# Performance work log

Measured on AMD Instinct MI355X. Metric: run time of the kernel, lower is better.

Reference implementation:

```python
import jax, jax.numpy as jnp
import numpy as np

N, E, C, L, H = 32768, 524288, 128, 3, 4
B, S = 64, 512            # graphs, nodes per graph (N = B*S, equal-size graphs)
F_X, F_PE = 64, 16
IN_DIM = F_X + F_PE
HID, OUT = 256, 1
EPS = 1e-5                # BatchNorm1d eps
HD = C // H               # head dim


def setup_inputs():
    key = jax.random.key(0)
    ks = iter(jax.random.split(key, 32))
    rn = lambda shape, s=0.05: jax.random.normal(next(ks), shape, dtype=jnp.float32) * s
    return dict(
        x=jax.random.normal(next(ks), (N, F_X), dtype=jnp.float32),
        pe=jax.random.normal(next(ks), (N, F_PE), dtype=jnp.float32),
        edge_index=jax.random.randint(next(ks), (2, E), 0, N),
        batch=jnp.repeat(jnp.arange(B), S),
        W_emb=rn((IN_DIM, C)), b_emb=jnp.zeros((C,), jnp.float32),
        gcn_w=rn((L, C, C)), gcn_b=jnp.zeros((L, C), jnp.float32),
        in_w=rn((L, 3 * C, C)), in_b=jnp.zeros((L, 3 * C), jnp.float32),
        out_w=rn((L, C, C)), out_b=jnp.zeros((L, C), jnp.float32),
        mlp_w1=rn((L, C, 2 * C)), mlp_b1=jnp.zeros((L, 2 * C), jnp.float32),
        mlp_w2=rn((L, 2 * C, C)), mlp_b2=jnp.zeros((L, C), jnp.float32),
        g1=jnp.ones((L, C), jnp.float32), be1=jnp.zeros((L, C), jnp.float32),
        g2=jnp.ones((L, C), jnp.float32), be2=jnp.zeros((L, C), jnp.float32),
        g3=jnp.ones((L, C), jnp.float32), be3=jnp.zeros((L, C), jnp.float32),
        W_hid=rn((C, HID)), b_hid=jnp.zeros((HID,), jnp.float32),
        W_out=rn((HID, OUT)), b_out=jnp.zeros((OUT,), jnp.float32),
    )


def _bn(h, g, b):
    # BatchNorm1d over nodes (training-mode batch stats, biased var)
    mu = h.mean(0)
    var = h.var(0)
    return (h - mu) * jax.lax.rsqrt(var + EPS) * g + b


def _gelu(x):
    return jax.nn.gelu(x, approximate=False)  # torch F.gelu default is erf


def reference(x, pe, edge_index, batch, W_emb, b_emb, gcn_w, gcn_b, in_w, in_b,
              out_w, out_b, mlp_w1, mlp_b1, mlp_w2, mlp_b2, g1, be1, g2, be2,
              g3, be3, W_hid, b_hid, W_out, b_out):
    # GCN normalization with self-loops (computed once; topology fixed)
    loops = jnp.arange(N)
    src = jnp.concatenate([edge_index[0], loops])
    dst = jnp.concatenate([edge_index[1], loops])
    deg = jax.ops.segment_sum(jnp.ones_like(src, jnp.float32), dst, num_segments=N)
    dinv = jnp.where(deg > 0, jax.lax.rsqrt(deg), 0.0)
    coef = (dinv[src] * dinv[dst])[:, None]

    h = jnp.concatenate([x, pe], axis=-1) @ W_emb + b_emb  # [N,C]
    scale = jnp.asarray(1.0 / np.sqrt(HD), jnp.float32)

    for l in range(L):
        # --- local GCNConv + residual + BN ---
        xw = h @ gcn_w[l]
        loc = jax.ops.segment_sum(xw[src] * coef, dst, num_segments=N) + gcn_b[l]
        h1 = _bn(loc + h, g1[l], be1[l])
        # --- global multihead attention on dense batch [B,S,C] ---
        hd = h.reshape(B, S, C)
        qkv = hd @ in_w[l].T + in_b[l]
        q, k, v = jnp.split(qkv, 3, axis=-1)
        sh = lambda t: t.reshape(B, S, H, HD).transpose(0, 2, 1, 3)  # [B,H,S,HD]
        q, k, v = sh(q), sh(k), sh(v)
        att = jax.nn.softmax(jnp.einsum('bhqd,bhkd->bhqk', q, k) * scale, axis=-1)
        ao = jnp.einsum('bhqk,bhkd->bhqd', att, v).transpose(0, 2, 1, 3).reshape(N, C)
        ao = ao @ out_w[l].T + out_b[l]
        h2 = _bn(ao + h, g2[l], be2[l])
        # --- combine + MLP residual + BN, then outer GELU ---
        out = h1 + h2
        m = jax.nn.relu(out @ mlp_w1[l] + mlp_b1[l]) @ mlp_w2[l] + mlp_b2[l]
        h = _gelu(_bn(out + m, g3[l], be3[l]))

    # global mean pool over graphs
    cnt = jax.ops.segment_sum(jnp.ones((N,), jnp.float32), batch, num_segments=B)
    pooled = jax.ops.segment_sum(h, batch, num_segments=B) / cnt[:, None]
    z = _gelu(pooled @ W_hid + b_hid)
    return (z @ W_out + b_out).squeeze()  # [B]
```

## Files before the change

kernel.cpp:

```cpp
#include <hip/hip_runtime.h>
#include <hip/hip_bf16.h>
#include <math.h>

#define NNODES 32768
#define NEDGES 524288
#define CCH 128
#define NLAYERS 3
#define NHEADS 4
#define HDIM 32
#define NB_GRAPH 64
#define SNODES 512
#define INDIM 80
#define HIDDEN 256
#define BNEPS 1e-5f

typedef _Float16 f16;
typedef f16 half8_t __attribute__((ext_vector_type(8)));
typedef f16 half4_t __attribute__((ext_vector_type(4)));
typedef float float4_t __attribute__((ext_vector_type(4)));

__device__ __forceinline__ float gelu_f(float x) {
    return 0.5f * x * (1.0f + erff(x * 0.70710678118654752f));
}

__global__ void k_count(const int* __restrict__ dst, int* __restrict__ deg) {
    int e = blockIdx.x * blockDim.x + threadIdx.x;
    if (e < NEDGES) atomicAdd(&deg[dst[e]], 1);
}

__global__ void k_dinv_from_deg(const int* __restrict__ deg, float* __restrict__ dinv) {
    int i = blockIdx.x * blockDim.x + threadIdx.x;
    if (i < NNODES) dinv[i] = rsqrtf((float)(deg[i] + 1));
}

__global__ __launch_bounds__(1024) void k_scan(const int* __restrict__ deg,
                                               int* __restrict__ rowptr,
                                               int* __restrict__ cursor) {
    __shared__ int sa[1024], sb[1024];
    int t = threadIdx.x;
    int base = t * 32;
    int local[32];
    int s = 0;
    #pragma unroll
    for (int i = 0; i < 32; i++) { local[i] = s; s += deg[base + i]; }
    sa[t] = s;
    __syncthreads();
    int* sp = sa; int* dp = sb;
    for (int off = 1; off < 1024; off <<= 1) {
        dp[t] = (t >= off) ? sp[t] + sp[t - off] : sp[t];
        __syncthreads();
        int* tmp = sp; sp = dp; dp = tmp;
    }
    int excl = (t == 0) ? 0 : sp[t - 1];
    #pragma unroll
    for (int i = 0; i < 32; i++) {
        int v = excl + local[i];
        rowptr[base + i] = v;
        cursor[base + i] = v;
    }
    if (t == 1023) rowptr[NNODES] = sp[1023];
}

__global__ void k_fill_edges(const int* __restrict__ src, const int* __restrict__ dst,
                             int* __restrict__ cursor, int* __restrict__ col) {
    int e = blockIdx.x * blockDim.x + threadIdx.x;
    if (e >= NEDGES) return;
    int pos = atomicAdd(&cursor[dst[e]], 1);
    col[pos] = src[e];
}

__global__ void k_concat(const float* __restrict__ x, const float* __restrict__ pe,
                         float* __restrict__ out) {
    int gid = blockIdx.x * blockDim.x + threadIdx.x;
    if (gid >= NNODES * 32) return;
    int n = gid >> 5, q = gid & 31;
    float4 v = {0.f, 0.f, 0.f, 0.f};
    if (q < 16)      v = ((const float4*)x)[(size_t)n * 16 + q];
    else if (q < 20) v = ((const float4*)pe)[(size_t)n * 4 + (q - 16)];
    ((float4*)out)[gid] = v;
}

__global__ void k_wconv(const float* __restrict__ src, f16* __restrict__ hi,
                        f16* __restrict__ lo, int Nn, int Ks, int Kp, int trans,
                        int L, int ostride) {
    int gid = blockIdx.x * blockDim.x + threadIdx.x;
    int per = Nn * Kp;
    if (gid >= per * L) return;
    int l = gid / per, r = gid % per;
    int n = r / Kp, k = r % Kp;
    float v = 0.f;
    if (k < Ks)
        v = trans ? src[(size_t)l * Nn * Ks + (size_t)n * Ks + k]
                  : src[(size_t)l * Ks * Nn + (size_t)k * Nn + n];
    f16 h = (f16)v;
    size_t o = (size_t)l * ostride + r;
    hi[o] = h;
    lo[o] = (f16)(v - (float)h);
}

template<int ACT, bool SPLIT>
__global__ __launch_bounds__(256) void k_gemm_mfma(
        const float* __restrict__ A, const f16* __restrict__ Whi,
        const f16* __restrict__ Wlo, const float* __restrict__ bias,
        const float* __restrict__ rowscale, float* __restrict__ C,
        int M, int N, int K, float* __restrict__ C2,
        const float* __restrict__ bias2) {
    __shared__ f16 Ah[128 * 40];
    __shared__ f16 Al[128 * 40];
    __shared__ f16 Bh[128 * 40];
    __shared__ f16 Bl[128 * 40];
    const int t = threadIdx.x;
    const int bm = blockIdx.y * 128, bn = blockIdx.x * 128;
    const int w = t >> 6, lane = t & 63;
    const int g = lane >> 4, q = lane & 15;

    float4_t acc[2][8];
    #pragma unroll
    for (int mt = 0; mt < 2; mt++)
        #pragma unroll
        for (int nt = 0; nt < 8; nt++)
            acc[mt][nt] = (float4_t){0.f, 0.f, 0.f, 0.f};

    const int srow = t >> 1, shf = (t & 1) * 16;

    for (int kc = 0; kc < K; kc += 32) {
        {
            const float* ap = A + (size_t)(bm + srow) * K + kc + shf;
            float va[16];
            *(float4*)&va[0]  = ((const float4*)ap)[0];
            *(float4*)&va[4]  = ((const float4*)ap)[1];
            *(float4*)&va[8]  = ((const float4*)ap)[2];
            *(float4*)&va[12] = ((const float4*)ap)[3];
            half8_t h0, h1, l0, l1;
            #pragma unroll
            for (int j = 0; j < 8; j++) {
                f16 h = (f16)va[j];
                h0[j] = h; l0[j] = (f16)(va[j] - (float)h);
            }
            #pragma unroll
            for (int j = 0; j < 8; j++) {
                f16 h = (f16)va[8 + j];
                h1[j] = h; l1[j] = (f16)(va[8 + j] - (float)h);
            }
            *(half8_t*)&Ah[srow * 40 + shf]     = h0;
            *(half8_t*)&Ah[srow * 40 + shf + 8] = h1;
            *(half8_t*)&Al[srow * 40 + shf]     = l0;
            *(half8_t*)&Al[srow * 40 + shf + 8] = l1;
        }
        {
            const f16* bp = Whi + (size_t)(bn + srow) * K + kc + shf;
            *(half8_t*)&Bh[srow * 40 + shf]     = ((const half8_t*)bp)[0];
            *(half8_t*)&Bh[srow * 40 + shf + 8] = ((const half8_t*)bp)[1];
            const f16* lp = Wlo + (size_t)(bn + srow) * K + kc + shf;
            *(half8_t*)&Bl[srow * 40 + shf]     = ((const half8_t*)lp)[0];
            *(half8_t*)&Bl[srow * 40 + shf + 8] = ((const half8_t*)lp)[1];
        }
        __syncthreads();

        half8_t ah[2], al[2];
        #pragma unroll
        for (int mt = 0; mt < 2; mt++) {
            ah[mt] = *(half8_t*)&Ah[(w * 32 + mt * 16 + q) * 40 + g * 8];
            al[mt] = *(half8_t*)&Al[(w * 32 + mt * 16 + q) * 40 + g * 8];
        }
        #pragma unroll
        for (int nt = 0; nt < 8; nt++) {
            half8_t bh = *(half8_t*)&Bh[(nt * 16 + q) * 40 + g * 8];
            half8_t bl = *(half8_t*)&Bl[(nt * 16 + q) * 40 + g * 8];
            #pragma unroll
            for (int mt = 0; mt < 2; mt++) {
                acc[mt][nt] = __builtin_amdgcn_mfma_f32_16x16x32_f16(ah[mt], bh, acc[mt][nt], 0, 0, 0);
                acc[mt][nt] = __builtin_amdgcn_mfma_f32_16x16x32_f16(al[mt], bh, acc[mt][nt], 0, 0, 0);
                acc[mt][nt] = __builtin_amdgcn_mfma_f32_16x16x32_f16(ah[mt], bl, acc[mt][nt], 0, 0, 0);
            }
        }
        __syncthreads();
    }

    #pragma unroll
    for (int mt = 0; mt < 2; mt++) {
        #pragma unroll
        for (int r = 0; r < 4; r++) {
            int row = bm + w * 32 + mt * 16 + 4 * g + r;
            if constexpr (SPLIT) {
                if (blockIdx.x == 0) {
                    float rs = rowscale[row];
                    #pragma unroll
                    for (int nt = 0; nt < 8; nt++) {
                        int cn = bn + nt * 16 + q;
                        C[(size_t)row * 128 + cn] = acc[mt][nt][r] * rs;
                    }
                } else {
                    #pragma unroll
                    for (int nt = 0; nt < 8; nt++) {
                        int cn2 = bn - 128 + nt * 16 + q;
                        C2[(size_t)row * 384 + cn2] = acc[mt][nt][r] + bias2[cn2];
                    }
                }
            } else {
                float rs = rowscale ? rowscale[row] : 1.0f;
                #pragma unroll
                for (int nt = 0; nt < 8; nt++) {
                    int cn = bn + nt * 16 + q;
                    float v = acc[mt][nt][r] + (bias ? bias[cn] : 0.0f);
                    v *= rs;
                    if (ACT == 1) v = fmaxf(v, 0.0f);
                    C[(size_t)row * N + cn] = v;
                }
            }
        }
    }
}

__global__ __launch_bounds__(256) void k_gcn_gather(
        const int* __restrict__ rowptr, const int* __restrict__ col,
        const float* __restrict__ xws, const float* __restrict__ dinv,
        const float* __restrict__ bias, float* __restrict__ loc) {
    int t = threadIdx.x;
    int node = blockIdx.x * 8 + (t >> 5);
    int q = t & 31;
    int r0 = rowptr[node], r1 = rowptr[node + 1];
    float4 acc = ((const float4*)(xws + (size_t)node * CCH))[q];
    for (int j = r0; j < r1; j++) {
        int s = col[j];
        float4 v = ((const float4*)(xws + (size_t)s * CCH))[q];
        acc.x += v.x; acc.y += v.y; acc.z += v.z; acc.w += v.w;
    }
    float dv = dinv[node];
    float4 b4 = ((const float4*)bias)[q];
    float4 o;
    o.x = fmaf(acc.x, dv, b4.x); o.y = fmaf(acc.y, dv, b4.y);
    o.z = fmaf(acc.z, dv, b4.z); o.w = fmaf(acc.w, dv, b4.w);
    ((float4*)(loc + (size_t)node * CCH))[q] = o;
}

__global__ __launch_bounds__(256) void k_bn_stats(const float* __restrict__ a,
                                                  const float* __restrict__ b,
                                                  float* __restrict__ part) {
    __shared__ float s1[256], s2[256];
    int t = threadIdx.x, blk = blockIdx.x;
    int c = t & 127, half = t >> 7;
    float sum = 0.f, sq = 0.f;
    for (int i = 0; i < 128; i++) {
        size_t r = (size_t)blk * 256 + half + 2 * i;
        float v = a[r * CCH + c] + b[r * CCH + c];
        sum += v;
        sq = fmaf(v, v, sq);
    }
    s1[t] = sum; s2[t] = sq;
    __syncthreads();
    if (t < 128) {
        part[blk * 256 + t]       = s1[t] + s1[t + 128];
        part[blk * 256 + 128 + t] = s2[t] + s2[t + 128];
    }
}

__global__ void k_bn_finalize(const float* __restrict__ part, const float* __restrict__ g,
                              const float* __restrict__ be, float* __restrict__ sc,
                              float* __restrict__ sh) {
    int c = threadIdx.x;
    float s = 0.f, sq = 0.f;
    for (int bk = 0; bk < 128; bk++) {
        s  += part[bk * 256 + c];
        sq += part[bk * 256 + 128 + c];
    }
    float mu = s / (float)NNODES;
    float var = sq / (float)NNODES - mu * mu;
    float rs = rsqrtf(var + BNEPS);
    float gg = g[c] * rs;
    sc[c] = gg;
    sh[c] = be[c] - mu * gg;
}

template<int ACT>
__global__ void k_bn_apply(const float* __restrict__ a, const float* __restrict__ b,
                           const float* __restrict__ sc, const float* __restrict__ sh,
                           float* __restrict__ out) {
    int gid = blockIdx.x * blockDim.x + threadIdx.x;
    if (gid >= NNODES * 32) return;
    int c = (gid & 31) * 4;
    float4 av = ((const float4*)a)[gid];
    float4 bv = ((const float4*)b)[gid];
    float r[4];
    float xs[4] = {av.x + bv.x, av.y + bv.y, av.z + bv.z, av.w + bv.w};
    #pragma unroll
    for (int j = 0; j < 4; j++) {
        float v = fmaf(xs[j], sc[c + j], sh[c + j]);
        if (ACT == 2) v = gelu_f(v);
        r[j] = v;
    }
    float4 o = {r[0], r[1], r[2], r[3]};
    ((float4*)out)[gid] = o;
}

__global__ void k_bn_apply_add(const float* __restrict__ a, const float* __restrict__ b,
                               const float* __restrict__ sc, const float* __restrict__ sh,
                               float* __restrict__ io) {
    int gid = blockIdx.x * blockDim.x + threadIdx.x;
    if (gid >= NNODES * 32) return;
    int c = (gid & 31) * 4;
    float4 av = ((const float4*)a)[gid];
    float4 bv = ((const float4*)b)[gid];
    float4 ov = ((const float4*)io)[gid];
    float xs[4] = {av.x + bv.x, av.y + bv.y, av.z + bv.z, av.w + bv.w};
    float r[4] = {ov.x, ov.y, ov.z, ov.w};
    #pragma unroll
    for (int j = 0; j < 4; j++) r[j] += fmaf(xs[j], sc[c + j], sh[c + j]);
    float4 o = {r[0], r[1], r[2], r[3]};
    ((float4*)io)[gid] = o;
}

__global__ __launch_bounds__(256, 1) void k_attn_mfma(const float* __restrict__ qkv,
                                                      float* __restrict__ ao) {
    __shared__ f16 Ks[512 * 40];
    __shared__ f16 VT[32 * 512];
    const int bh = blockIdx.x;
    const int b = bh >> 2, hh = bh & 3;
    const int t = threadIdx.x;
    const int lane = t & 63, wave = t >> 6;
    const int g = lane >> 4, q16 = lane & 15;
    const float scale = 0.17677669529663689f;

    const float* base = qkv + (size_t)b * SNODES * 384;

    #pragma unroll
    for (int it = 0; it < 8; it++) {
        int u = it * 256 + t;
        int row = u >> 2, c = u & 3;
        const float* gp = base + (size_t)row * 384 + CCH + hh * HDIM + c * 8;
        float4 v0 = *(const float4*)gp;
        float4 v1 = *(const float4*)(gp + 4);
        half8_t hv;
        hv[0] = (f16)v0.x; hv[1] = (f16)v0.y; hv[2] = (f16)v0.z; hv[3] = (f16)v0.w;
        hv[4] = (f16)v1.x; hv[5] = (f16)v1.y; hv[6] = (f16)v1.z; hv[7] = (f16)v1.w;
        *(half8_t*)(Ks + row * 40 + c * 8) = hv;
    }

    #pragma unroll
    for (int it = 0; it < 16; it++) {
        int j4 = (t >> 3) & 3;
        int n  = it * 32 + ((t >> 5) & 7) * 4 + j4;
        int c  = t & 7;
        float4 v = *(const float4*)(base + (size_t)n * 384 + 2 * CCH + hh * HDIM + c * 4);
        float4 u1;
        u1.x = __shfl_xor(v.x, 8); u1.y = __shfl_xor(v.y, 8);
        u1.z = __shfl_xor(v.z, 8); u1.w = __shfl_xor(v.w, 8);
        float4 w;
        if ((t & 8) == 0) { w.x = v.x;  w.y = u1.x; w.z = v.z;  w.w = u1.z; }
        else              { w.x = u1.y; w.y = v.y;  w.z = u1.w; w.w = v.w;  }
        float4 u2;
        u2.x = __shfl_xor(w.x, 16); u2.y = __shfl_xor(w.y, 16);
        u2.z = __shfl_xor(w.z, 16); u2.w = __shfl_xor(w.w, 16);
        float4 o;
        if ((t & 16) == 0) { o.x = w.x;  o.y = w.y;  o.z = u2.x; o.w = u2.y; }
        else               { o.x = u2.z; o.y = u2.w; o.z = w.z;  o.w = w.w;  }
        int hd = c * 4 + j4;
        int n0 = it * 32 + ((t >> 5) & 7) * 4;
        half4_t pk;
        pk[0] = (f16)o.x; pk[1] = (f16)o.y; pk[2] = (f16)o.z; pk[3] = (f16)o.w;
        int pos = ((n0 >> 2) + hd) & 127;
        *(half4_t*)(VT + hd * 512 + pos * 4) = pk;
    }
    __syncthreads();

    for (int j = 0; j < 8; j++) {
        int qt = wave * 8 + j;

        const float* qp = base + (size_t)(qt * 16 + q16) * 384 + hh * HDIM + g * 8;
        float4 q0 = *(const float4*)qp;
        float4 q1 = *(const float4*)(qp + 4);
        half8_t qf;
        qf[0] = (f16)(q0.x * scale); qf[1] = (f16)(q0.y * scale);
        qf[2] = (f16)(q0.z * scale); qf[3] = (f16)(q0.w * scale);
        qf[4] = (f16)(q1.x * scale); qf[5] = (f16)(q1.y * scale);
        qf[6] = (f16)(q1.z * scale); qf[7] = (f16)(q1.w * scale);

        float4_t acc[32];
        #pragma unroll
        for (int kt = 0; kt < 32; kt++) {
            half8_t kf = *(half8_t*)(Ks + (kt * 16 + q16) * 40 + g * 8);
            float4_t z = {0.f, 0.f, 0.f, 0.f};
            acc[kt] = __builtin_amdgcn_mfma_f32_16x16x32_f16(kf, qf, z, 0, 0, 0);
        }

        float m = -1e30f;
        #pragma unroll
        for (int kt = 0; kt < 32; kt++)
            m = fmaxf(m, fmaxf(fmaxf(acc[kt][0], acc[kt][1]),
                               fmaxf(acc[kt][2], acc[kt][3])));
        m = fmaxf(m, __shfl_xor(m, 16));
        m = fmaxf(m, __shfl_xor(m, 32));
        float s = 0.f;
        #pragma unroll
        for (int kt = 0; kt < 32; kt++) {
            acc[kt][0] = __expf(acc[kt][0] - m);
            acc[kt][1] = __expf(acc[kt][1] - m);
            acc[kt][2] = __expf(acc[kt][2] - m);
            acc[kt][3] = __expf(acc[kt][3] - m);
            s += acc[kt][0] + acc[kt][1] + acc[kt][2] + acc[kt][3];
        }
        s += __shfl_xor(s, 16);
        s += __shfl_xor(s, 32);
        float inv = 1.0f / s;

        half8_t pa[16];
        #pragma unroll
        for (int T = 0; T < 16; T++) {
            pa[T][0] = (f16)(acc[2 * T][0] * inv);
            pa[T][1] = (f16)(acc[2 * T][1] * inv);
            pa[T][2] = (f16)(acc[2 * T][2] * inv);
            pa[T][3] = (f16)(acc[2 * T][3] * inv);
            pa[T][4] = (f16)(acc[2 * T + 1][0] * inv);
            pa[T][5] = (f16)(acc[2 * T + 1][1] * inv);
            pa[T][6] = (f16)(acc[2 * T + 1][2] * inv);
            pa[T][7] = (f16)(acc[2 * T + 1][3] * inv);
        }

        float4_t oa0 = {0.f, 0.f, 0.f, 0.f}, oa1 = {0.f, 0.f, 0.f, 0.f};
        #pragma unroll
        for (int T = 0; T < 16; T++) {
            int hd0 = q16;
            half4_t b00 = *(half4_t*)(VT + hd0 * 512 + (((8 * T + g + hd0) & 127) * 4));
            half4_t b01 = *(half4_t*)(VT + hd0 * 512 + (((8 * T + 4 + g + hd0) & 127) * 4));
            half8_t vb0;
            vb0[0] = b00[0]; vb0[1] = b00[1]; vb0[2] = b00[2]; vb0[3] = b00[3];
            vb0[4] = b01[0]; vb0[5] = b01[1]; vb0[6] = b01[2]; vb0[7] = b01[3];
            oa0 = __builtin_amdgcn_mfma_f32_16x16x32_f16(pa[T], vb0, oa0, 0, 0, 0);
            int hd1 = 16 + q16;
            half4_t b10 = *(half4_t*)(VT + hd1 * 512 + (((8 * T + g + hd1) & 127) * 4));
            half4_t b11 = *(half4_t*)(VT + hd1 * 512 + (((8 * T + 4 + g + hd1) & 127) * 4));
            half8_t vb1;
            vb1[0] = b10[0]; vb1[1] = b10[1]; vb1[2] = b10[2]; vb1[3] = b10[3];
            vb1[4] = b11[0]; vb1[5] = b11[1]; vb1[6] = b11[2]; vb1[7] = b11[3];
            oa1 = __builtin_amdgcn_mfma_f32_16x16x32_f16(pa[T], vb1, oa1, 0, 0, 0);
        }

        #pragma unroll
        for (int r = 0; r < 4; r++) {
            size_t row = (size_t)(b * SNODES + qt * 16 + 4 * g + r);
            ao[row * CCH + hh * HDIM + q16]      = oa0[r];
            ao[row * CCH + hh * HDIM + 16 + q16] = oa1[r];
        }
    }
}

__global__ __launch_bounds__(256) void k_pool2(const float* __restrict__ h,
                                               const int* __restrict__ batch,
                                               float* __restrict__ pooled,
                                               float* __restrict__ cnt) {
    __shared__ float bins[NB_GRAPH * 132];
    __shared__ int cbin[NB_GRAPH];
    int t = threadIdx.x;
    for (int i = t; i < NB_GRAPH * 132; i += 256) bins[i] = 0.f;
    if (t < NB_GRAPH) cbin[t] = 0;
    __syncthreads();
    int n0 = blockIdx.x * 256;
    int c = t & 127, half = t >> 7;
    for (int i = 0; i < 128; i++) {
        int n = n0 + 2 * i + half;
        int g = batch[n];
        atomicAdd(&bins[g * 132 + c], h[(size_t)n * CCH + c]);
        if (c == 0) atomicAdd(&cbin[g], 1);
    }
    __syncthreads();
    for (int i = t; i < NB_GRAPH * CCH; i += 256) {
        int g = i >> 7, cc = i & 127;
        float v = bins[g * 132 + cc];
        if (v != 0.f) atomicAdd(&pooled[g * CCH + cc], v);
    }
    if (t < NB_GRAPH && cbin[t]) atomicAdd(&cnt[t], (float)cbin[t]);
}

__global__ __launch_bounds__(256) void k_head(const float* __restrict__ pooled,
                                              const float* __restrict__ cnt,
                                              const float* __restrict__ Wh,
                                              const float* __restrict__ bh,
                                              const float* __restrict__ Wo,
                                              const float* __restrict__ bo,
                                              float* __restrict__ out) {
    __shared__ float p[128];
    __shared__ float red[256];
    int g = blockIdx.x, t = threadIdx.x;
    if (t < 128) p[t] = pooled[g * CCH + t] / cnt[g];
    __syncthreads();
    float a = bh[t];
    for (int k = 0; k < 128; k++) a = fmaf(p[k], Wh[k * HIDDEN + t], a);
    float z = gelu_f(a);
    red[t] = z * Wo[t];
    __syncthreads();
    for (int s = 128; s > 0; s >>= 1) {
        if (t < s) red[t] += red[t + s];
        __syncthreads();
    }
    if (t == 0) out[g] = red[0] + bo[0];
}

extern "C" void kernel_launch(void* const* d_in, const int* in_sizes, int n_in,
                              void* d_out, int out_size, void* d_ws, size_t ws_size,
                              hipStream_t stream) {
    const float* x      = (const float*)d_in[0];
    const float* pe     = (const float*)d_in[1];
    const int*   ei     = (const int*)d_in[2];
    const int*   batch  = (const int*)d_in[3];
    const float* W_emb  = (const float*)d_in[4];
    const float* b_emb  = (const float*)d_in[5];
    const float* gcn_w  = (const float*)d_in[6];
    const float* gcn_b  = (const float*)d_in[7];
    const float* in_w   = (const float*)d_in[8];
    const float* in_b   = (const float*)d_in[9];
    const float* out_w  = (const float*)d_in[10];
    const float* out_b  = (const float*)d_in[11];
    const float* mlp_w1 = (const float*)d_in[12];
    const float* mlp_b1 = (const float*)d_in[13];
    const float* mlp_w2 = (const float*)d_in[14];
    const float* mlp_b2 = (const float*)d_in[15];
    const float* g1     = (const float*)d_in[16];
    const float* be1    = (const float*)d_in[17];
    const float* g2     = (const float*)d_in[18];
    const float* be2    = (const float*)d_in[19];
    const float* g3     = (const float*)d_in[20];
    const float* be3    = (const float*)d_in[21];
    const float* W_hid  = (const float*)d_in[22];
    const float* b_hid  = (const float*)d_in[23];
    const float* W_out  = (const float*)d_in[24];
    const float* b_out  = (const float*)d_in[25];
    float* out = (float*)d_out;

    float* ws = (float*)d_ws;
    const size_t NC = (size_t)NNODES * CCH;
    float* dinv   = ws;
    float* h      = dinv + NNODES;
    float* A      = h + NC;
    float* Bb     = A + NC;
    float* qkv    = Bb + NC;
    float* part   = qkv + (size_t)NNODES * 384;
    float* sc     = part + 128 * 256;
    float* sh     = sc + CCH;
    float* pooled = sh + CCH;
    float* cnt    = pooled + (size_t)NB_GRAPH * CCH;
    int*   ideg   = (int*)(cnt + NB_GRAPH);
    int*   rowptr = ideg + NNODES;
    int*   cursor = rowptr + NNODES + 1;
    int*   col    = cursor + NNODES;
    f16* wb    = (f16*)(col + NEDGES);
    f16* embh  = wb;                      f16* embl = embh + 128 * 128;
    f16* cwh   = embl + 128 * 128;        f16* cwl  = cwh + 3 * 512 * 128;
    f16* outh  = cwl + 3 * 512 * 128;     f16* outl = outh + 3 * 128 * 128;
    f16* m1h   = outl + 3 * 128 * 128;    f16* m1l  = m1h + 3 * 256 * 128;
    f16* m2h   = m1l + 3 * 256 * 128;     f16* m2l  = m2h + 3 * 128 * 256;

    const int* srcp = ei;
    const int* dstp = ei + NEDGES;

    const int NC4 = NNODES * 32;

    hipMemsetAsync(ideg, 0, NNODES * sizeof(int), stream);
    k_count<<<NEDGES / 256, 256, 0, stream>>>(dstp, ideg);
    k_dinv_from_deg<<<NNODES / 256, 256, 0, stream>>>(ideg, dinv);
    k_scan<<<1, 1024, 0, stream>>>(ideg, rowptr, cursor);
    k_fill_edges<<<NEDGES / 256, 256, 0, stream>>>(srcp, dstp, cursor, col);

    k_wconv<<<(128 * 128 + 255) / 256, 256, 0, stream>>>(W_emb, embh, embl, 128, 80, 128, 0, 1, 128 * 128);
    k_wconv<<<(3 * 128 * 128 + 255) / 256, 256, 0, stream>>>(gcn_w, cwh, cwl, 128, 128, 128, 0, 3, 512 * 128);
    k_wconv<<<(3 * 384 * 128 + 255) / 256, 256, 0, stream>>>(in_w, cwh + 128 * 128, cwl + 128 * 128, 384, 128, 128, 1, 3, 512 * 128);
    k_wconv<<<(3 * 128 * 128 + 255) / 256, 256, 0, stream>>>(out_w, outh, outl, 128, 128, 128, 1, 3, 128 * 128);
    k_wconv<<<(3 * 256 * 128 + 255) / 256, 256, 0, stream>>>(mlp_w1, m1h, m1l, 256, 128, 128, 0, 3, 256 * 128);
    k_wconv<<<(3 * 128 * 256 + 255) / 256, 256, 0, stream>>>(mlp_w2, m2h, m2l, 128, 256, 256, 0, 3, 128 * 256);

    k_concat<<<NC4 / 256, 256, 0, stream>>>(x, pe, A);
    k_gemm_mfma<0, false><<<dim3(1, NNODES / 128), 256, 0, stream>>>(
        A, embh, embl, b_emb, nullptr, h, NNODES, CCH, 128, nullptr, nullptr);

    for (int l = 0; l < NLAYERS; l++) {
        k_gemm_mfma<0, true><<<dim3(4, NNODES / 128), 256, 0, stream>>>(
            h, cwh + (size_t)l * 512 * 128, cwl + (size_t)l * 512 * 128,
            nullptr, dinv, A, NNODES, 512, 128, qkv, in_b + l * 384);
        k_gcn_gather<<<NNODES / 8, 256, 0, stream>>>(
            rowptr, col, A, dinv, gcn_b + l * CCH, Bb);
        k_bn_stats<<<128, 256, 0, stream>>>(Bb, h, part);
        k_bn_finalize<<<1, 128, 0, stream>>>(part, g1 + l * CCH, be1 + l * CCH, sc, sh);
        k_bn_apply<0><<<NC4 / 256, 256, 0, stream>>>(Bb, h, sc, sh, A);

        k_attn_mfma<<<NB_GRAPH * NHEADS, 256, 0, stream>>>(qkv, Bb);
        k_gemm_mfma<0, false><<<dim3(1, NNODES / 128), 256, 0, stream>>>(
            Bb, outh + (size_t)l * 128 * 128, outl + (size_t)l * 128 * 128,
            out_b + l * CCH, nullptr, qkv, NNODES, CCH, 128, nullptr, nullptr);
        k_bn_stats<<<128, 256, 0, stream>>>(qkv, h, part);
        k_bn_finalize<<<1, 128, 0, stream>>>(part, g2 + l * CCH, be2 + l * CCH, sc, sh);
        k_bn_apply_add<<<NC4 / 256, 256, 0, stream>>>(qkv, h, sc, sh, A);

        k_gemm_mfma<1, false><<<dim3(2, NNODES / 128), 256, 0, stream>>>(
            A, m1h + (size_t)l * 256 * 128, m1l + (size_t)l * 256 * 128,
            mlp_b1 + l * 256, nullptr, qkv, NNODES, 256, 128, nullptr, nullptr);
        k_gemm_mfma<0, false><<<dim3(1, NNODES / 128), 256, 0, stream>>>(
            qkv, m2h + (size_t)l * 128 * 256, m2l + (size_t)l * 128 * 256,
            mlp_b2 + l * CCH, nullptr, Bb, NNODES, CCH, 256, nullptr, nullptr);
        k_bn_stats<<<128, 256, 0, stream>>>(A, Bb, part);
        k_bn_finalize<<<1, 128, 0, stream>>>(part, g3 + l * CCH, be3 + l * CCH, sc, sh);
        k_bn_apply<2><<<NC4 / 256, 256, 0, stream>>>(A, Bb, sc, sh, h);
    }

    hipMemsetAsync(pooled, 0, ((size_t)NB_GRAPH * CCH + NB_GRAPH) * sizeof(float), stream);
    k_pool2<<<NNODES / 256, 256, 0, stream>>>(h, batch, pooled, cnt);
    k_head<<<NB_GRAPH, 256, 0, stream>>>(pooled, cnt, W_hid, b_hid, W_out, b_out, out);
}
```

Measured before the change: 953.2 us.

## Use online-softmax chunked attention with 512-thread blocks

Replaces the full-row softmax (32 MFMA accumulators held live per query tile) with a flash-style online softmax over four key chunks of 128, rescaling the output accumulators as the running max changes. This cuts register pressure. The block doubles to 512 threads (8 waves), each handling four query tiles, and the K/V shared-memory staging loops are adjusted to match. It adds rescaling exps and shuffles per chunk. The 256 blocks still leave many CUs at one block each, so the gain would come mainly from more waves per block hiding latency.

Measured after the change: 897.8 us. -5.8%, faster.

```diff
diff --git a/kernel.cpp b/kernel.cpp
--- a/kernel.cpp
+++ b/kernel.cpp
@@ -310,8 +310,8 @@
     ((float4*)io)[gid] = o;
 }
 
-__global__ __launch_bounds__(256, 1) void k_attn_mfma(const float* __restrict__ qkv,
-                                                      float* __restrict__ ao) {
+__global__ __launch_bounds__(512) void k_attn_flash(const float* __restrict__ qkv,
+                                                    float* __restrict__ ao) {
     __shared__ f16 Ks[512 * 40];
     __shared__ f16 VT[32 * 512];
     const int bh = blockIdx.x;
@@ -324,8 +324,8 @@
     const float* base = qkv + (size_t)b * SNODES * 384;
 
     #pragma unroll
-    for (int it = 0; it < 8; it++) {
-        int u = it * 256 + t;
+    for (int it = 0; it < 4; it++) {
+        int u = it * 512 + t;
         int row = u >> 2, c = u & 3;
         const float* gp = base + (size_t)row * 384 + CCH + hh * HDIM + c * 8;
         float4 v0 = *(const float4*)gp;
@@ -337,9 +337,9 @@
     }
 
     #pragma unroll
-    for (int it = 0; it < 16; it++) {
+    for (int it = 0; it < 8; it++) {
         int j4 = (t >> 3) & 3;
-        int n  = it * 32 + ((t >> 5) & 7) * 4 + j4;
+        int n  = it * 64 + ((t >> 5) & 15) * 4 + j4;
         int c  = t & 7;
         float4 v = *(const float4*)(base + (size_t)n * 384 + 2 * CCH + hh * HDIM + c * 4);
         float4 u1;
@@ -355,7 +355,7 @@
         if ((t & 16) == 0) { o.x = w.x;  o.y = w.y;  o.z = u2.x; o.w = u2.y; }
         else               { o.x = u2.z; o.y = u2.w; o.z = w.z;  o.w = w.w;  }
         int hd = c * 4 + j4;
-        int n0 = it * 32 + ((t >> 5) & 7) * 4;
+        int n0 = it * 64 + ((t >> 5) & 15) * 4;
         half4_t pk;
         pk[0] = (f16)o.x; pk[1] = (f16)o.y; pk[2] = (f16)o.z; pk[3] = (f16)o.w;
         int pos = ((n0 >> 2) + hd) & 127;
@@ -363,8 +363,8 @@
     }
     __syncthreads();
 
-    for (int j = 0; j < 8; j++) {
-        int qt = wave * 8 + j;
+    for (int j = 0; j < 4; j++) {
+        int qt = wave * 4 + j;
 
         const float* qp = base + (size_t)(qt * 16 + q16) * 384 + hh * HDIM + g * 8;
         float4 q0 = *(const float4*)qp;
@@ -375,71 +375,79 @@
         qf[4] = (f16)(q1.x * scale); qf[5] = (f16)(q1.y * scale);
         qf[6] = (f16)(q1.z * scale); qf[7] = (f16)(q1.w * scale);
 
-        float4_t acc[32];
-        #pragma unroll
-        for (int kt = 0; kt < 32; kt++) {
-            half8_t kf = *(half8_t*)(Ks + (kt * 16 + q16) * 40 + g * 8);
-            float4_t z = {0.f, 0.f, 0.f, 0.f};
-            acc[kt] = __builtin_amdgcn_mfma_f32_16x16x32_f16(kf, qf, z, 0, 0, 0);
+        float m = -1e30f, l = 0.f;
+        float4_t oa0 = {0.f, 0.f, 0.f, 0.f}, oa1 = {0.f, 0.f, 0.f, 0.f};
+
+        for (int ci = 0; ci < 4; ci++) {
+            float4_t acc[8];
+            #pragma unroll
+            for (int ktl = 0; ktl < 8; ktl++) {
+                half8_t kf = *(half8_t*)(Ks + ((ci * 8 + ktl) * 16 + q16) * 40 + g * 8);
+                float4_t z = {0.f, 0.f, 0.f, 0.f};
+                acc[ktl] = __builtin_amdgcn_mfma_f32_16x16x32_f16(kf, qf, z, 0, 0, 0);
+            }
+
+            float cm = -1e30f;
+            #pragma unroll
+            for (int ktl = 0; ktl < 8; ktl++)
+                cm = fmaxf(cm, fmaxf(fmaxf(acc[ktl][0], acc[ktl][1]),
+                                     fmaxf(acc[ktl][2], acc[ktl][3])));
+            cm = fmaxf(cm, __shfl_xor(cm, 16));
+            cm = fmaxf(cm, __shfl_xor(cm, 32));
+
+            float mn = fmaxf(m, cm);
+            float scq = __expf(m - mn);
+            m = mn;
+            l *= scq;
+            #pragma unroll
+            for (int r = 0; r < 4; r++) {
+                float scr = __shfl(scq, 4 * g + r);
+                oa0[r] *= scr;
+                oa1[r] *= scr;
+            }
+
+            half8_t pa[4];
+            #pragma unroll
+            for (int Tl = 0; Tl < 4; Tl++) {
+                #pragma unroll
+                for (int i = 0; i < 4; i++) {
+                    float e0 = __expf(acc[2 * Tl][i] - m);
+                    float e1 = __expf(acc[2 * Tl + 1][i] - m);
+                    l += e0 + e1;
+                    pa[Tl][i]     = (f16)e0;
+                    pa[Tl][4 + i] = (f16)e1;
+                }
+            }
+
+            #pragma unroll
+            for (int Tl = 0; Tl < 4; Tl++) {
+                int T = ci * 4 + Tl;
+                int hd0 = q16;
+                half4_t b00 = *(half4_t*)(VT + hd0 * 512 + (((8 * T + g + hd0) & 127) * 4));
+                half4_t b01 = *(half4_t*)(VT + hd0 * 512 + (((8 * T + 4 + g + hd0) & 127) * 4));
+                half8_t vb0;
+                vb0[0] = b00[0]; vb0[1] = b00[1]; vb0[2] = b00[2]; vb0[3] = b00[3];
+                vb0[4] = b01[0]; vb0[5] = b01[1]; vb0[6] = b01[2]; vb0[7] = b01[3];
+                oa0 = __builtin_amdgcn_mfma_f32_16x16x32_f16(pa[Tl], vb0, oa0, 0, 0, 0);
+                int hd1 = 16 + q16;
+                half4_t b10 = *(half4_t*)(VT + hd1 * 512 + (((8 * T + g + hd1) & 127) * 4));
+                half4_t b11 = *(half4_t*)(VT + hd1 * 512 + (((8 * T + 4 + g + hd1) & 127) * 4));
+                half8_t vb1;
+                vb1[0] = b10[0]; vb1[1] = b10[1]; vb1[2] = b10[2]; vb1[3] = b10[3];
+                vb1[4] = b11[0]; vb1[5] = b11[1]; vb1[6] = b11[2]; vb1[7] = b11[3];
+                oa1 = __builtin_amdgcn_mfma_f32_16x16x32_f16(pa[Tl], vb1, oa1, 0, 0, 0);
+            }
         }
 
-        float m = -1e30f;
-        #pragma unroll
-        for (int kt = 0; kt < 32; kt++)
-            m = fmaxf(m, fmaxf(fmaxf(acc[kt][0], acc[kt][1]),
-                               fmaxf(acc[kt][2], acc[kt][3])));
-        m = fmaxf(m, __shfl_xor(m, 16));
-        m = fmaxf(m, __shfl_xor(m, 32));
-        float s = 0.f;
-        #pragma unroll
-        for (int kt = 0; kt < 32; kt++) {
-            acc[kt][0] = __expf(acc[kt][0] - m);
-            acc[kt][1] = __expf(acc[kt][1] - m);
-            acc[kt][2] = __expf(acc[kt][2] - m);
-            acc[kt][3] = __expf(acc[kt][3] - m);
-            s += acc[kt][0] + acc[kt][1] + acc[kt][2] + acc[kt][3];
-        }
-        s += __shfl_xor(s, 16);
-        s += __shfl_xor(s, 32);
-        float inv = 1.0f / s;
-
-        half8_t pa[16];
-        #pragma unroll
-        for (int T = 0; T < 16; T++) {
-            pa[T][0] = (f16)(acc[2 * T][0] * inv);
-            pa[T][1] = (f16)(acc[2 * T][1] * inv);
-            pa[T][2] = (f16)(acc[2 * T][2] * inv);
-            pa[T][3] = (f16)(acc[2 * T][3] * inv);
-            pa[T][4] = (f16)(acc[2 * T + 1][0] * inv);
-            pa[T][5] = (f16)(acc[2 * T + 1][1] * inv);
-            pa[T][6] = (f16)(acc[2 * T + 1][2] * inv);
-            pa[T][7] = (f16)(acc[2 * T + 1][3] * inv);
-        }
-
-        float4_t oa0 = {0.f, 0.f, 0.f, 0.f}, oa1 = {0.f, 0.f, 0.f, 0.f};
-        #pragma unroll
-        for (int T = 0; T < 16; T++) {
-            int hd0 = q16;
-            half4_t b00 = *(half4_t*)(VT + hd0 * 512 + (((8 * T + g + hd0) & 127) * 4));
-            half4_t b01 = *(half4_t*)(VT + hd0 * 512 + (((8 * T + 4 + g + hd0) & 127) * 4));
-            half8_t vb0;
-            vb0[0] = b00[0]; vb0[1] = b00[1]; vb0[2] = b00[2]; vb0[3] = b00[3];
-            vb0[4] = b01[0]; vb0[5] = b01[1]; vb0[6] = b01[2]; vb0[7] = b01[3];
-            oa0 = __builtin_amdgcn_mfma_f32_16x16x32_f16(pa[T], vb0, oa0, 0, 0, 0);
-            int hd1 = 16 + q16;
-            half4_t b10 = *(half4_t*)(VT + hd1 * 512 + (((8 * T + g + hd1) & 127) * 4));
-            half4_t b11 = *(half4_t*)(VT + hd1 * 512 + (((8 * T + 4 + g + hd1) & 127) * 4));
-            half8_t vb1;
-            vb1[0] = b10[0]; vb1[1] = b10[1]; vb1[2] = b10[2]; vb1[3] = b10[3];
-            vb1[4] = b11[0]; vb1[5] = b11[1]; vb1[6] = b11[2]; vb1[7] = b11[3];
-            oa1 = __builtin_amdgcn_mfma_f32_16x16x32_f16(pa[T], vb1, oa1, 0, 0, 0);
-        }
-
+        l += __shfl_xor(l, 16);
+        l += __shfl_xor(l, 32);
+        float invq = 1.0f / l;
         #pragma unroll
         for (int r = 0; r < 4; r++) {
+            float invr = __shfl(invq, 4 * g + r);
             size_t row = (size_t)(b * SNODES + qt * 16 + 4 * g + r);
-            ao[row * CCH + hh * HDIM + q16]      = oa0[r];
-            ao[row * CCH + hh * HDIM + 16 + q16] = oa1[r];
+            ao[row * CCH + hh * HDIM + q16]      = oa0[r] * invr;
+            ao[row * CCH + hh * HDIM + 16 + q16] = oa1[r] * invr;
         }
     }
 }
@@ -581,7 +589,7 @@
         k_bn_finalize<<<1, 128, 0, stream>>>(part, g1 + l * CCH, be1 + l * CCH, sc, sh);
         k_bn_apply<0><<<NC4 / 256, 256, 0, stream>>>(Bb, h, sc, sh, A);
 
-        k_attn_mfma<<<NB_GRAPH * NHEADS, 256, 0, stream>>>(qkv, Bb);
+        k_attn_flash<<<NB_GRAPH * NHEADS, 512, 0, stream>>>(qkv, Bb);
         k_gemm_mfma<0, false><<<dim3(1, NNODES / 128), 256, 0, stream>>>(
             Bb, outh + (size_t)l * 128 * 128, outl + (size_t)l * 128 * 128,
             out_b + l * CCH, nullptr, qkv, NNODES, CCH, 128, nullptr, nullptr);
```
